# Kernel tuning notes

Measured on AMD Instinct MI355X. Metric: run time of the kernel, lower is better.

Reference implementation:

```python
import jax, jax.numpy as jnp
import numpy as np

D_MODEL, D_K, D_V, H = 1024, 64, 64, 16
B, NQ, NK = 2, 2048, 2048


def setup_inputs() -> dict:
    key = jax.random.key(0)
    ks = jax.random.split(key, 12)
    hd = H * D_K
    xav = lambda k, shape: jax.random.uniform(k, shape, jnp.float32, -1.0, 1.0) * np.sqrt(6.0 / (shape[0] + shape[1]))
    return {
        "queries": jax.random.normal(ks[0], (B, NQ, D_MODEL), jnp.float32),
        "keys": jax.random.normal(ks[1], (B, NK, D_MODEL), jnp.float32),
        "values": jax.random.normal(ks[2], (B, NK, D_MODEL), jnp.float32),
        "memory": jax.random.uniform(ks[3], (B, NK), jnp.float32),
        "Wq": xav(ks[4], (D_MODEL, hd)), "bq": jnp.zeros((hd,), jnp.float32),
        "Wk": xav(ks[5], (D_MODEL, hd)), "bk": jnp.zeros((hd,), jnp.float32),
        "Wv": xav(ks[6], (D_MODEL, H * D_V)), "bv": jnp.zeros((H * D_V,), jnp.float32),
        "Wo": xav(ks[7], (H * D_V, D_MODEL)), "bo": jnp.zeros((D_MODEL,), jnp.float32),
        "Wmm": xav(ks[8], (1, H * D_V)), "bmm": jnp.zeros((H * D_V,), jnp.float32),
    }


def reference(queries, keys, values, memory, Wq, bq, Wk, bk, Wv, bv, Wo, bo, Wmm, bmm):
    b, nq = queries.shape[:2]
    nk = keys.shape[1]
    # projections -> (b, h, n, d)
    q = (queries @ Wq + bq).reshape(b, nq, H, D_K).transpose(0, 2, 1, 3)
    k = (keys @ Wk + bk).reshape(b, nk, H, D_K).transpose(0, 2, 1, 3)
    v = (values @ Wv + bv).reshape(b, nk, H, D_V).transpose(0, 2, 1, 3)
    # memory gate: fc_mm(memory[..., None]) -> (b, nk, h*d_k) -> (b, h, nk, d_k)
    mm = (memory[:, :, None] * Wmm[0] + bmm).reshape(b, nk, H, D_K).transpose(0, 2, 1, 3)
    att = jnp.einsum("bhqd,bhkd->bhqk", q, k * mm) / np.sqrt(D_K).astype(np.float32)
    att = jax.nn.softmax(att, axis=-1)
    out = jnp.einsum("bhqk,bhkd->bhqd", att, v * mm)
    out = out.transpose(0, 2, 1, 3).reshape(b, nq, H * D_V)
    return out @ Wo + bo
```

## Files before the change

### kernel.cpp

```cpp
#include <hip/hip_runtime.h>
#include <hip/hip_bf16.h>

#define H_   16
#define NQ_  2048
#define NK_  2048
#define DM_  1024

typedef float f32x4 __attribute__((ext_vector_type(4)));
typedef float f32x16 __attribute__((ext_vector_type(16)));
typedef __bf16 bf16x8 __attribute__((ext_vector_type(8)));
typedef unsigned short u16x8 __attribute__((ext_vector_type(8)));
typedef unsigned short u16x4 __attribute__((ext_vector_type(4)));

__device__ __forceinline__ unsigned short bfbits(float x) {
  __bf16 h = (__bf16)x;
  return __builtin_bit_cast(unsigned short, h);
}

__global__ __launch_bounds__(256) void prep(
    const float* __restrict__ Wq, const float* __restrict__ Wk,
    const float* __restrict__ Wv, const float* __restrict__ Wo,
    unsigned short* __restrict__ WqT, unsigned short* __restrict__ WkT,
    unsigned short* __restrict__ WvT, unsigned short* __restrict__ WoT,
    const float* __restrict__ q, const float* __restrict__ k, const float* __restrict__ v,
    unsigned short* __restrict__ qo, unsigned short* __restrict__ ko,
    unsigned short* __restrict__ vo) {
  __shared__ float t[64][65];
  const int flat = blockIdx.x;
  if (flat < 1024) {
    const int z = flat >> 8, bx = (flat >> 4) & 15, by = flat & 15;
    const float* src = (z == 0) ? Wq : (z == 1) ? Wk : (z == 2) ? Wv : Wo;
    unsigned short* dst = (z == 0) ? WqT : (z == 1) ? WkT : (z == 2) ? WvT : WoT;
    const int r0 = bx * 64, c0 = by * 64;
    for (int i = threadIdx.x; i < 4096; i += 256) {
      int r = i >> 6, c = i & 63;
      t[r][c] = src[(size_t)(r0 + r) * DM_ + c0 + c];
    }
    __syncthreads();
    for (int i = threadIdx.x; i < 4096; i += 256) {
      int n = i >> 6, kk = i & 63;
      dst[(size_t)(c0 + n) * DM_ + r0 + kk] = bfbits(t[kk][n]);
    }
  } else {
    const int tt = flat - 1024;
    const int which = tt >> 11;
    const float* src = (which == 0) ? q : (which == 1) ? k : v;
    unsigned short* dst = (which == 0) ? qo : (which == 1) ? ko : vo;
    const int i = (tt & 2047) * 256 + threadIdx.x;
    const float4* s4 = (const float4*)src;
    float4 a = s4[2 * i], b = s4[2 * i + 1];
    bf16x8 o;
    o[0] = (__bf16)a.x; o[1] = (__bf16)a.y; o[2] = (__bf16)a.z; o[3] = (__bf16)a.w;
    o[4] = (__bf16)b.x; o[5] = (__bf16)b.y; o[6] = (__bf16)b.z; o[7] = (__bf16)b.w;
    *((bf16x8*)dst + i) = o;
  }
}

__device__ __forceinline__ void gll16(const unsigned short* g, unsigned short* l) {
  __builtin_amdgcn_global_load_lds((const __attribute__((address_space(1))) void*)g,
                                   (__attribute__((address_space(3))) void*)l, 16, 0, 0);
}

template <int MODE>
__device__ __forceinline__ void gemm128_body(
    int bx, int by,
    const unsigned short* __restrict__ A, const unsigned short* __restrict__ Bt, int K,
    const float* __restrict__ bias, const float* __restrict__ mem,
    const float* __restrict__ Wmm, const float* __restrict__ bmm,
    unsigned short* __restrict__ obf,
    unsigned short* Al, unsigned short* Bl) {
  const int tid = threadIdx.x, lane = tid & 63, w = tid >> 6;
  const int wm = w >> 1, wn = w & 1;
  const int m0 = bx * 128, n0 = by * 128;
  const int lrow = lane >> 2, lcol = (lane & 3) * 8;
  const int fr = lane & 15, fk = (lane >> 4) * 8;

  f32x4 acc[4][4] = {};

  const unsigned short* ag0 = A + (size_t)(m0 + w * 32 + lrow) * K + lcol;
  const unsigned short* bg0 = Bt + (size_t)(n0 + w * 32 + lrow) * K + lcol;
  unsigned short* la0 = &Al[(w * 32) * 32];
  unsigned short* la1 = &Al[(w * 32 + 16) * 32];
  unsigned short* lb0 = &Bl[(w * 32) * 32];
  unsigned short* lb1 = &Bl[(w * 32 + 16) * 32];
  const size_t s16K = (size_t)16 * K;

  const int KT = K >> 5;
  for (int kt = 0; kt < KT; ++kt) {
    gll16(ag0, la0); gll16(ag0 + s16K, la1);
    gll16(bg0, lb0); gll16(bg0 + s16K, lb1);
    ag0 += 32; bg0 += 32;
    __syncthreads();
    bf16x8 af[4], bfr[4];
#pragma unroll
    for (int i = 0; i < 4; ++i) af[i] = *(const bf16x8*)&Al[(wm * 64 + i * 16 + fr) * 32 + fk];
#pragma unroll
    for (int j = 0; j < 4; ++j) bfr[j] = *(const bf16x8*)&Bl[(wn * 64 + j * 16 + fr) * 32 + fk];
#pragma unroll
    for (int i = 0; i < 4; ++i)
#pragma unroll
      for (int j = 0; j < 4; ++j)
        acc[i][j] = __builtin_amdgcn_mfma_f32_16x16x32_bf16(af[i], bfr[j], acc[i][j], 0, 0, 0);
    __syncthreads();
  }

#pragma unroll
  for (int i = 0; i < 4; ++i) {
    const int rowb = m0 + wm * 64 + i * 16 + (lane >> 4) * 4;
#pragma unroll
    for (int j = 0; j < 4; ++j) {
      const int col = n0 + wn * 64 + j * 16 + fr;
#pragma unroll
      for (int r = 0; r < 4; ++r) {
        float v = acc[i][j][r];
        int rr = rowb + r;
        if (MODE == 0) {
          int b = rr >> 11, nq = rr & 2047, h = col >> 6, d = col & 63;
          float val = (v + bias[col]) * 0.180336884f;
          obf[(((size_t)(b * H_ + h)) * NQ_ + nq) * 64 + d] = bfbits(val);
        } else if (MODE == 1) {
          int b = rr >> 11, nk = rr & 2047, h = col >> 6, d = col & 63;
          float gate = mem[b * NK_ + nk] * Wmm[col] + bmm[col];
          float val = (v + bias[col]) * gate;
          obf[(((size_t)(b * H_ + h)) * NK_ + nk) * 64 + d] = bfbits(val);
        } else {
          int b = col >> 11, key = col & 2047, h = rr >> 6, d = rr & 63;
          float gate = mem[b * NK_ + key] * Wmm[rr] + bmm[rr];
          float val = (v + bias[rr]) * gate;
          int keyp = (key & ~12) | ((key & 4) << 1) | ((key & 8) >> 1);
          obf[(((size_t)(b * H_ + h)) * 64 + d) * NK_ + keyp] = bfbits(val);
        }
      }
    }
  }
}

__global__ __launch_bounds__(256) void gemm_qkv3(
    const unsigned short* __restrict__ qbf, const unsigned short* __restrict__ kbf,
    const unsigned short* __restrict__ vbf, const unsigned short* __restrict__ WvT,
    const unsigned short* __restrict__ WqT, const unsigned short* __restrict__ WkT,
    const float* __restrict__ bq, const float* __restrict__ bk, const float* __restrict__ bv,
    const float* __restrict__ mem, const float* __restrict__ Wmm, const float* __restrict__ bmm,
    unsigned short* __restrict__ Qp, unsigned short* __restrict__ Kp,
    unsigned short* __restrict__ VpT) {
  __shared__ unsigned short Al[128 * 32];
  __shared__ unsigned short Bl[128 * 32];
  const int gid = (blockIdx.x & 7) * 96 + (blockIdx.x >> 3);
  if (gid < 256) {
    gemm128_body<0>(gid & 31, gid >> 5, qbf, WqT, 1024, bq, nullptr, nullptr, nullptr,
                    Qp, Al, Bl);
  } else if (gid < 512) {
    int bb = gid - 256;
    gemm128_body<1>(bb & 31, bb >> 5, kbf, WkT, 1024, bk, mem, Wmm, bmm, Kp, Al, Bl);
  } else {
    int bb = gid - 512;
    gemm128_body<2>(bb & 7, bb >> 3, WvT, vbf, 1024, bv, mem, Wmm, bmm, VpT, Al, Bl);
  }
}

__global__ __launch_bounds__(256) void gemm_out(
    const unsigned short* __restrict__ AO, const unsigned short* __restrict__ WoT,
    const float* __restrict__ bo, float* __restrict__ out) {
  __shared__ unsigned short Al[64 * 32];
  __shared__ unsigned short Bl[128 * 32];
  const int b = (blockIdx.x & 7) * 64 + (blockIdx.x >> 3);
  const int bx = b & 63, by = b >> 6;
  const int tid = threadIdx.x, lane = tid & 63, w = tid >> 6;
  const int wm = w >> 1, wn = w & 1;
  const int m0 = bx * 64, n0 = by * 128;
  const int lrow = lane >> 2, lcol = (lane & 3) * 8;
  const int fr = lane & 15, fk = (lane >> 4) * 8;
  const int K = 1024;

  f32x4 acc[2][4] = {};

  const unsigned short* ag = AO + (size_t)(m0 + w * 16 + lrow) * K + lcol;
  const unsigned short* bg = WoT + (size_t)(n0 + w * 32 + lrow) * K + lcol;
  unsigned short* la0 = &Al[(w * 16) * 32];
  unsigned short* lb0 = &Bl[(w * 32) * 32];
  unsigned short* lb1 = &Bl[(w * 32 + 16) * 32];
  const size_t s16K = (size_t)16 * K;

  for (int kt = 0; kt < 32; ++kt) {
    gll16(ag, la0);
    gll16(bg, lb0); gll16(bg + s16K, lb1);
    ag += 32; bg += 32;
    __syncthreads();
    bf16x8 af[2], bfr[4];
#pragma unroll
    for (int i = 0; i < 2; ++i) af[i] = *(const bf16x8*)&Al[(wm * 32 + i * 16 + fr) * 32 + fk];
#pragma unroll
    for (int j = 0; j < 4; ++j) bfr[j] = *(const bf16x8*)&Bl[(wn * 64 + j * 16 + fr) * 32 + fk];
#pragma unroll
    for (int i = 0; i < 2; ++i)
#pragma unroll
      for (int j = 0; j < 4; ++j)
        acc[i][j] = __builtin_amdgcn_mfma_f32_16x16x32_bf16(af[i], bfr[j], acc[i][j], 0, 0, 0);
    __syncthreads();
  }

#pragma unroll
  for (int i = 0; i < 2; ++i) {
    const int rowb = m0 + wm * 32 + i * 16 + (lane >> 4) * 4;
#pragma unroll
    for (int j = 0; j < 4; ++j) {
      const int col = n0 + wn * 64 + j * 16 + fr;
#pragma unroll
      for (int r = 0; r < 4; ++r)
        out[(size_t)(rowb + r) * DM_ + col] = acc[i][j][r] + bo[col];
    }
  }
}

__global__ __launch_bounds__(256, 2) void flash_attn(const unsigned short* __restrict__ Qp,
                                                     const unsigned short* __restrict__ Kp,
                                                     const unsigned short* __restrict__ VpT,
                                                     unsigned short* __restrict__ AO) {
  __shared__ unsigned short Ks[2][128][66];
  __shared__ unsigned short Vs[2][64][130];

  const int tid = threadIdx.x, lane = tid & 63, w = tid >> 6;
  const int gid = (blockIdx.x & 7) * 64 + (blockIdx.x >> 3);
  const int bh = gid >> 4;
  const int qt = gid & 15;
  const int r31 = lane & 31, hi2 = lane >> 5;

  const unsigned short* qg = Qp + (((size_t)bh * NQ_) + qt * 128 + w * 32 + r31) * 64 + hi2 * 8;
  bf16x8 qf[4];
#pragma unroll
  for (int s = 0; s < 4; ++s) qf[s] = *(const bf16x8*)&qg[s * 16];

  const int krow = tid >> 1, kcol = (tid & 1) * 32;
  const int vrow = tid >> 2, vcol = (tid & 3) * 32;
  const unsigned short* kg = Kp + ((size_t)bh * NK_ + krow) * 64 + kcol;
  const unsigned short* vg = VpT + ((size_t)bh * 64 + vrow) * NK_ + vcol;

  f32x16 acc0 = {}, acc1 = {};
  float m_run = -1e30f, l_run = 0.0f;

  u16x8 kr[4], vr[4];
#pragma unroll
  for (int i = 0; i < 4; ++i) {
    kr[i] = *(const u16x8*)(kg + 8 * i);
    vr[i] = *(const u16x8*)(vg + 8 * i);
  }
#pragma unroll
  for (int i = 0; i < 4; ++i) {
    *(u16x8*)&Ks[0][krow][kcol + 8 * i] = kr[i];
    *(u16x8*)&Vs[0][vrow][vcol + 8 * i] = vr[i];
  }

  for (int kt = 0; kt < 16; ++kt) {
    const int cur = kt & 1;
    __syncthreads();

    f32x16 sv[4] = {};
    __builtin_amdgcn_s_setprio(1);
#pragma unroll
    for (int s = 0; s < 4; ++s) {
#pragma unroll
      for (int kb = 0; kb < 4; ++kb) {
        bf16x8 ka = *(const bf16x8*)&Ks[cur][kb * 32 + r31][s * 16 + hi2 * 8];
        sv[kb] = __builtin_amdgcn_mfma_f32_32x32x16_bf16(ka, qf[s], sv[kb], 0, 0, 0);
      }
    }
    __builtin_amdgcn_s_setprio(0);

    if (kt + 1 < 16) {
      const unsigned short* kn = kg + (size_t)(kt + 1) * 128 * 64;
      const unsigned short* vn = vg + (kt + 1) * 128;
#pragma unroll
      for (int i = 0; i < 4; ++i) {
        kr[i] = *(const u16x8*)(kn + 8 * i);
        vr[i] = *(const u16x8*)(vn + 8 * i);
      }
    }

    float mxp[4];
#pragma unroll
    for (int kb = 0; kb < 4; ++kb) {
      float m = fmaxf(sv[kb][0], sv[kb][1]);
#pragma unroll
      for (int g = 2; g < 16; ++g) m = fmaxf(m, sv[kb][g]);
      mxp[kb] = m;
    }
    float mx = fmaxf(fmaxf(mxp[0], mxp[1]), fmaxf(mxp[2], mxp[3]));
    mx = fmaxf(mx, __shfl_xor(mx, 32));

    if (__any(mx > m_run + 8.0f)) {
      float mnew = fmaxf(m_run, mx);
      float sc = __builtin_amdgcn_exp2f(m_run - mnew);
      m_run = mnew;
      l_run *= sc;
      acc0 *= sc;
      acc1 *= sc;
    }

    float psp[4] = {0.f, 0.f, 0.f, 0.f};
    bf16x8 pb[8];
#pragma unroll
    for (int kb = 0; kb < 4; ++kb) {
#pragma unroll
      for (int g = 0; g < 16; ++g) {
        float p = __builtin_amdgcn_exp2f(sv[kb][g] - m_run);
        psp[kb] += p;
        pb[2 * kb + (g >> 3)][g & 7] = (__bf16)p;
      }
    }
    float ps = (psp[0] + psp[1]) + (psp[2] + psp[3]);
    ps += __shfl_xor(ps, 32);
    l_run += ps;

    __builtin_amdgcn_s_setprio(1);
#pragma unroll
    for (int ks = 0; ks < 8; ++ks) {
      bf16x8 va0 = *(const bf16x8*)&Vs[cur][r31][ks * 16 + hi2 * 8];
      bf16x8 va1 = *(const bf16x8*)&Vs[cur][32 + r31][ks * 16 + hi2 * 8];
      acc0 = __builtin_amdgcn_mfma_f32_32x32x16_bf16(va0, pb[ks], acc0, 0, 0, 0);
      acc1 = __builtin_amdgcn_mfma_f32_32x32x16_bf16(va1, pb[ks], acc1, 0, 0, 0);
    }
    __builtin_amdgcn_s_setprio(0);

    if (kt + 1 < 16) {
#pragma unroll
      for (int i = 0; i < 4; ++i) {
        *(u16x8*)&Ks[cur ^ 1][krow][kcol + 8 * i] = kr[i];
        *(u16x8*)&Vs[cur ^ 1][vrow][vcol + 8 * i] = vr[i];
      }
    }
  }

  const int b = bh >> 4, h = bh & 15;
  const float linv = 1.0f / l_run;
  const int qrow = qt * 128 + w * 32 + r31;
  const size_t rowbase = (((size_t)b * NQ_ + qrow) << 10) + h * 64;
#pragma unroll
  for (int c = 0; c < 4; ++c) {
    u16x4 o0, o1;
#pragma unroll
    for (int i = 0; i < 4; ++i) {
      o0[i] = bfbits(acc0[c * 4 + i] * linv);
      o1[i] = bfbits(acc1[c * 4 + i] * linv);
    }
    *(u16x4*)&AO[rowbase + 8 * c + 4 * hi2]      = o0;
    *(u16x4*)&AO[rowbase + 32 + 8 * c + 4 * hi2] = o1;
  }
}

extern "C" void kernel_launch(void* const* d_in, const int* in_sizes, int n_in,
                              void* d_out, int out_size, void* d_ws, size_t ws_size,
                              hipStream_t stream) {
  const float* queries = (const float*)d_in[0];
  const float* keys    = (const float*)d_in[1];
  const float* values  = (const float*)d_in[2];
  const float* memory  = (const float*)d_in[3];
  const float* Wq  = (const float*)d_in[4];
  const float* bq  = (const float*)d_in[5];
  const float* Wk  = (const float*)d_in[6];
  const float* bk  = (const float*)d_in[7];
  const float* Wv  = (const float*)d_in[8];
  const float* bv  = (const float*)d_in[9];
  const float* Wo  = (const float*)d_in[10];
  const float* bo  = (const float*)d_in[11];
  const float* Wmm = (const float*)d_in[12];
  const float* bmm = (const float*)d_in[13];

  char* ws = (char*)d_ws;
  const size_t SZ_X = (size_t)4096 * 1024 * 2;
  const size_t SZ_W = (size_t)1024 * 1024 * 2;
  unsigned short* qbf = (unsigned short*)(ws);
  unsigned short* kbf = (unsigned short*)(ws + SZ_X);
  unsigned short* vbf = (unsigned short*)(ws + 2 * SZ_X);
  unsigned short* AO  = (unsigned short*)(ws);
  size_t off = 3 * SZ_X;
  unsigned short* WqT = (unsigned short*)(ws + off); off += SZ_W;
  unsigned short* WkT = (unsigned short*)(ws + off); off += SZ_W;
  unsigned short* WvT = (unsigned short*)(ws + off); off += SZ_W;
  unsigned short* WoT = (unsigned short*)(ws + off); off += SZ_W;
  unsigned short* Qp  = (unsigned short*)(ws + off); off += SZ_X;
  unsigned short* Kp  = (unsigned short*)(ws + off); off += SZ_X;
  unsigned short* VpT = (unsigned short*)(ws + off); off += SZ_X;

  prep<<<7168, 256, 0, stream>>>(Wq, Wk, Wv, Wo, WqT, WkT, WvT, WoT,
                                 queries, keys, values, qbf, kbf, vbf);

  gemm_qkv3<<<768, 256, 0, stream>>>(qbf, kbf, vbf, WvT, WqT, WkT,
                                     bq, bk, bv, memory, Wmm, bmm, Qp, Kp, VpT);

  flash_attn<<<512, 256, 0, stream>>>(Qp, Kp, VpT, AO);

  gemm_out<<<512, 256, 0, stream>>>(AO, WoT, bo, (float*)d_out);
}
```

Baseline: 132.4 us.

## Split attention over two key halves and merge partial outputs

The attention kernel now splits the 2048 keys into two halves processed by separate blocks, which doubles the grid to 1024 blocks. It also halves the K/V shared-memory tile to 64 keys and raises the occupancy hint to 4 blocks per CU. Each block writes an unnormalized bf16 partial output plus its running max and sum. A new merge kernel combines the two halves with log-sum-exp weights. The aim is more parallelism and better latency hiding, paid for by an extra kernel launch, extra partial-output traffic, more barriers per key, and storing unnormalized partials in bf16.

After: 138.8 us. 4.8% more time.

```diff
diff --git a/kernel.cpp b/kernel.cpp
--- a/kernel.cpp
+++ b/kernel.cpp
@@ -15,6 +15,10 @@
 __device__ __forceinline__ unsigned short bfbits(float x) {
   __bf16 h = (__bf16)x;
   return __builtin_bit_cast(unsigned short, h);
+}
+__device__ __forceinline__ float bf2f(unsigned short h) {
+  unsigned int u = ((unsigned int)h) << 16;
+  return __builtin_bit_cast(float, u);
 }
 
 __global__ __launch_bounds__(256) void prep(
@@ -212,17 +216,19 @@
   }
 }
 
-__global__ __launch_bounds__(256, 2) void flash_attn(const unsigned short* __restrict__ Qp,
+__global__ __launch_bounds__(256, 4) void flash_attn(const unsigned short* __restrict__ Qp,
                                                      const unsigned short* __restrict__ Kp,
                                                      const unsigned short* __restrict__ VpT,
-                                                     unsigned short* __restrict__ AO) {
-  __shared__ unsigned short Ks[2][128][66];
-  __shared__ unsigned short Vs[2][64][130];
+                                                     unsigned short* __restrict__ Opart,
+                                                     float* __restrict__ ml) {
+  __shared__ unsigned short Ks[2][64][66];
+  __shared__ unsigned short Vs[2][64][66];
 
   const int tid = threadIdx.x, lane = tid & 63, w = tid >> 6;
-  const int gid = (blockIdx.x & 7) * 64 + (blockIdx.x >> 3);
-  const int bh = gid >> 4;
+  const int gid = (blockIdx.x & 7) * 128 + (blockIdx.x >> 3);
   const int qt = gid & 15;
+  const int bh = (gid >> 4) & 31;
+  const int half = gid >> 9;
   const int r31 = lane & 31, hi2 = lane >> 5;
 
   const unsigned short* qg = Qp + (((size_t)bh * NQ_) + qt * 128 + w * 32 + r31) * 64 + hi2 * 8;
@@ -230,61 +236,44 @@
 #pragma unroll
   for (int s = 0; s < 4; ++s) qf[s] = *(const bf16x8*)&qg[s * 16];
 
-  const int krow = tid >> 1, kcol = (tid & 1) * 32;
-  const int vrow = tid >> 2, vcol = (tid & 3) * 32;
-  const unsigned short* kg = Kp + ((size_t)bh * NK_ + krow) * 64 + kcol;
-  const unsigned short* vg = VpT + ((size_t)bh * 64 + vrow) * NK_ + vcol;
+  const int srow = tid >> 2, scol = (tid & 3) * 16;
+  const unsigned short* kg = Kp + ((size_t)bh * NK_ + half * 1024 + srow) * 64 + scol;
+  const unsigned short* vg = VpT + ((size_t)bh * 64 + srow) * NK_ + half * 1024 + scol;
 
   f32x16 acc0 = {}, acc1 = {};
   float m_run = -1e30f, l_run = 0.0f;
 
-  u16x8 kr[4], vr[4];
-#pragma unroll
-  for (int i = 0; i < 4; ++i) {
-    kr[i] = *(const u16x8*)(kg + 8 * i);
-    vr[i] = *(const u16x8*)(vg + 8 * i);
-  }
-#pragma unroll
-  for (int i = 0; i < 4; ++i) {
-    *(u16x8*)&Ks[0][krow][kcol + 8 * i] = kr[i];
-    *(u16x8*)&Vs[0][vrow][vcol + 8 * i] = vr[i];
-  }
+  u16x8 kr0 = *(const u16x8*)kg, kr1 = *(const u16x8*)(kg + 8);
+  u16x8 vr0 = *(const u16x8*)vg, vr1 = *(const u16x8*)(vg + 8);
+  *(u16x8*)&Ks[0][srow][scol] = kr0; *(u16x8*)&Ks[0][srow][scol + 8] = kr1;
+  *(u16x8*)&Vs[0][srow][scol] = vr0; *(u16x8*)&Vs[0][srow][scol + 8] = vr1;
 
   for (int kt = 0; kt < 16; ++kt) {
     const int cur = kt & 1;
     __syncthreads();
 
-    f32x16 sv[4] = {};
+    f32x16 sv0 = {}, sv1 = {};
     __builtin_amdgcn_s_setprio(1);
 #pragma unroll
     for (int s = 0; s < 4; ++s) {
-#pragma unroll
-      for (int kb = 0; kb < 4; ++kb) {
-        bf16x8 ka = *(const bf16x8*)&Ks[cur][kb * 32 + r31][s * 16 + hi2 * 8];
-        sv[kb] = __builtin_amdgcn_mfma_f32_32x32x16_bf16(ka, qf[s], sv[kb], 0, 0, 0);
-      }
+      bf16x8 ka0 = *(const bf16x8*)&Ks[cur][r31][s * 16 + hi2 * 8];
+      bf16x8 ka1 = *(const bf16x8*)&Ks[cur][32 + r31][s * 16 + hi2 * 8];
+      sv0 = __builtin_amdgcn_mfma_f32_32x32x16_bf16(ka0, qf[s], sv0, 0, 0, 0);
+      sv1 = __builtin_amdgcn_mfma_f32_32x32x16_bf16(ka1, qf[s], sv1, 0, 0, 0);
     }
     __builtin_amdgcn_s_setprio(0);
 
     if (kt + 1 < 16) {
-      const unsigned short* kn = kg + (size_t)(kt + 1) * 128 * 64;
-      const unsigned short* vn = vg + (kt + 1) * 128;
-#pragma unroll
-      for (int i = 0; i < 4; ++i) {
-        kr[i] = *(const u16x8*)(kn + 8 * i);
-        vr[i] = *(const u16x8*)(vn + 8 * i);
-      }
-    }
-
-    float mxp[4];
-#pragma unroll
-    for (int kb = 0; kb < 4; ++kb) {
-      float m = fmaxf(sv[kb][0], sv[kb][1]);
-#pragma unroll
-      for (int g = 2; g < 16; ++g) m = fmaxf(m, sv[kb][g]);
-      mxp[kb] = m;
-    }
-    float mx = fmaxf(fmaxf(mxp[0], mxp[1]), fmaxf(mxp[2], mxp[3]));
+      const unsigned short* kn = kg + (size_t)(kt + 1) * 64 * 64;
+      const unsigned short* vn = vg + (kt + 1) * 64;
+      kr0 = *(const u16x8*)kn; kr1 = *(const u16x8*)(kn + 8);
+      vr0 = *(const u16x8*)vn; vr1 = *(const u16x8*)(vn + 8);
+    }
+
+    float mA = fmaxf(sv0[0], sv0[1]), mB = fmaxf(sv1[0], sv1[1]);
+#pragma unroll
+    for (int g = 2; g < 16; ++g) { mA = fmaxf(mA, sv0[g]); mB = fmaxf(mB, sv1[g]); }
+    float mx = fmaxf(mA, mB);
     mx = fmaxf(mx, __shfl_xor(mx, 32));
 
     if (__any(mx > m_run + 8.0f)) {
@@ -296,24 +285,23 @@
       acc1 *= sc;
     }
 
-    float psp[4] = {0.f, 0.f, 0.f, 0.f};
-    bf16x8 pb[8];
-#pragma unroll
-    for (int kb = 0; kb < 4; ++kb) {
-#pragma unroll
-      for (int g = 0; g < 16; ++g) {
-        float p = __builtin_amdgcn_exp2f(sv[kb][g] - m_run);
-        psp[kb] += p;
-        pb[2 * kb + (g >> 3)][g & 7] = (__bf16)p;
-      }
-    }
-    float ps = (psp[0] + psp[1]) + (psp[2] + psp[3]);
+    float psA = 0.0f, psB = 0.0f;
+    bf16x8 pb[4];
+#pragma unroll
+    for (int g = 0; g < 16; ++g) {
+      float pA = __builtin_amdgcn_exp2f(sv0[g] - m_run);
+      float pB = __builtin_amdgcn_exp2f(sv1[g] - m_run);
+      psA += pA; psB += pB;
+      pb[g >> 3][g & 7] = (__bf16)pA;
+      pb[2 + (g >> 3)][g & 7] = (__bf16)pB;
+    }
+    float ps = psA + psB;
     ps += __shfl_xor(ps, 32);
     l_run += ps;
 
     __builtin_amdgcn_s_setprio(1);
 #pragma unroll
-    for (int ks = 0; ks < 8; ++ks) {
+    for (int ks = 0; ks < 4; ++ks) {
       bf16x8 va0 = *(const bf16x8*)&Vs[cur][r31][ks * 16 + hi2 * 8];
       bf16x8 va1 = *(const bf16x8*)&Vs[cur][32 + r31][ks * 16 + hi2 * 8];
       acc0 = __builtin_amdgcn_mfma_f32_32x32x16_bf16(va0, pb[ks], acc0, 0, 0, 0);
@@ -322,29 +310,54 @@
     __builtin_amdgcn_s_setprio(0);
 
     if (kt + 1 < 16) {
-#pragma unroll
-      for (int i = 0; i < 4; ++i) {
-        *(u16x8*)&Ks[cur ^ 1][krow][kcol + 8 * i] = kr[i];
-        *(u16x8*)&Vs[cur ^ 1][vrow][vcol + 8 * i] = vr[i];
-      }
+      *(u16x8*)&Ks[cur ^ 1][srow][scol] = kr0; *(u16x8*)&Ks[cur ^ 1][srow][scol + 8] = kr1;
+      *(u16x8*)&Vs[cur ^ 1][srow][scol] = vr0; *(u16x8*)&Vs[cur ^ 1][srow][scol + 8] = vr1;
     }
   }
 
   const int b = bh >> 4, h = bh & 15;
-  const float linv = 1.0f / l_run;
   const int qrow = qt * 128 + w * 32 + r31;
-  const size_t rowbase = (((size_t)b * NQ_ + qrow) << 10) + h * 64;
+  unsigned short* ob = Opart + (((size_t)half * 4096 + b * 2048 + qrow) << 10) + h * 64 + 4 * hi2;
 #pragma unroll
   for (int c = 0; c < 4; ++c) {
     u16x4 o0, o1;
 #pragma unroll
     for (int i = 0; i < 4; ++i) {
-      o0[i] = bfbits(acc0[c * 4 + i] * linv);
-      o1[i] = bfbits(acc1[c * 4 + i] * linv);
-    }
-    *(u16x4*)&AO[rowbase + 8 * c + 4 * hi2]      = o0;
-    *(u16x4*)&AO[rowbase + 32 + 8 * c + 4 * hi2] = o1;
-  }
+      o0[i] = bfbits(acc0[c * 4 + i]);
+      o1[i] = bfbits(acc1[c * 4 + i]);
+    }
+    *(u16x4*)(ob + 8 * c) = o0;
+    *(u16x4*)(ob + 32 + 8 * c) = o1;
+  }
+  if (hi2 == 0) {
+    float2 v; v.x = m_run; v.y = l_run;
+    *(float2*)&ml[(((size_t)half * 32 + bh) * 2048 + qrow) * 2] = v;
+  }
+}
+
+__global__ __launch_bounds__(256) void merge_halves(const unsigned short* __restrict__ Opart,
+                                                    const float* __restrict__ ml,
+                                                    unsigned short* __restrict__ AO) {
+  const int i = blockIdx.x * 256 + threadIdx.x;
+  const int row = i >> 7;
+  const int d8 = (i & 127) * 8;
+  const int b = row >> 11, q = row & 2047, h = d8 >> 6;
+  const int bh = b * 16 + h;
+  const unsigned short* p1 = Opart + ((size_t)row << 10) + d8;
+  const unsigned short* p2 = p1 + ((size_t)4096 << 10);
+  float2 ml1 = *(const float2*)&ml[((size_t)bh * 2048 + q) * 2];
+  float2 ml2 = *(const float2*)&ml[(((size_t)32 + bh) * 2048 + q) * 2];
+  float m = fmaxf(ml1.x, ml2.x);
+  float w1 = __builtin_amdgcn_exp2f(ml1.x - m);
+  float w2 = __builtin_amdgcn_exp2f(ml2.x - m);
+  float inv = 1.0f / (ml1.y * w1 + ml2.y * w2);
+  float s1 = w1 * inv, s2 = w2 * inv;
+  u16x8 a = *(const u16x8*)p1;
+  u16x8 c = *(const u16x8*)p2;
+  u16x8 o;
+#pragma unroll
+  for (int j = 0; j < 8; ++j) o[j] = bfbits(bf2f(a[j]) * s1 + bf2f(c[j]) * s2);
+  *(u16x8*)&AO[((size_t)row << 10) + d8] = o;
 }
 
 extern "C" void kernel_launch(void* const* d_in, const int* in_sizes, int n_in,
@@ -366,20 +379,20 @@
   const float* bmm = (const float*)d_in[13];
 
   char* ws = (char*)d_ws;
-  const size_t SZ_X = (size_t)4096 * 1024 * 2;
-  const size_t SZ_W = (size_t)1024 * 1024 * 2;
-  unsigned short* qbf = (unsigned short*)(ws);
-  unsigned short* kbf = (unsigned short*)(ws + SZ_X);
-  unsigned short* vbf = (unsigned short*)(ws + 2 * SZ_X);
-  unsigned short* AO  = (unsigned short*)(ws);
-  size_t off = 3 * SZ_X;
-  unsigned short* WqT = (unsigned short*)(ws + off); off += SZ_W;
-  unsigned short* WkT = (unsigned short*)(ws + off); off += SZ_W;
-  unsigned short* WvT = (unsigned short*)(ws + off); off += SZ_W;
-  unsigned short* WoT = (unsigned short*)(ws + off); off += SZ_W;
-  unsigned short* Qp  = (unsigned short*)(ws + off); off += SZ_X;
-  unsigned short* Kp  = (unsigned short*)(ws + off); off += SZ_X;
-  unsigned short* VpT = (unsigned short*)(ws + off); off += SZ_X;
+  const size_t MB = 1024 * 1024;
+  unsigned short* qbf   = (unsigned short*)(ws);
+  unsigned short* AO    = (unsigned short*)(ws);
+  unsigned short* kbf   = (unsigned short*)(ws + 8 * MB);
+  unsigned short* vbf   = (unsigned short*)(ws + 16 * MB);
+  unsigned short* Opart = (unsigned short*)(ws + 8 * MB);
+  float*          mlb   = (float*)(ws + 24 * MB);
+  unsigned short* WqT   = (unsigned short*)(ws + 26 * MB);
+  unsigned short* WkT   = (unsigned short*)(ws + 28 * MB);
+  unsigned short* WvT   = (unsigned short*)(ws + 30 * MB);
+  unsigned short* WoT   = (unsigned short*)(ws + 32 * MB);
+  unsigned short* Qp    = (unsigned short*)(ws + 34 * MB);
+  unsigned short* Kp    = (unsigned short*)(ws + 42 * MB);
+  unsigned short* VpT   = (unsigned short*)(ws + 50 * MB);
 
   prep<<<7168, 256, 0, stream>>>(Wq, Wk, Wv, Wo, WqT, WkT, WvT, WoT,
                                  queries, keys, values, qbf, kbf, vbf);
@@ -387,7 +400,9 @@
   gemm_qkv3<<<768, 256, 0, stream>>>(qbf, kbf, vbf, WvT, WqT, WkT,
                                      bq, bk, bv, memory, Wmm, bmm, Qp, Kp, VpT);
 
-  flash_attn<<<512, 256, 0, stream>>>(Qp, Kp, VpT, AO);
+  flash_attn<<<1024, 256, 0, stream>>>(Qp, Kp, VpT, Opart, mlb);
+
+  merge_halves<<<2048, 256, 0, stream>>>(Opart, mlb, AO);
 
   gemm_out<<<512, 256, 0, stream>>>(AO, WoT, bo, (float*)d_out);
 }
```

## Double-buffer LDS tiles in projection GEMMs to overlap loads with MFMA

Applied to the files above, without the earlier changes.

Both the QKV projection GEMM and the output GEMM now use two LDS buffers per operand. The next K-tile is fetched with global_load_lds before the MFMAs on the current tile run, so global-memory latency can hide behind compute instead of stalling at a barrier every iteration. This doubles LDS use per block, which may reduce occupancy. Overlap depends on the trailing barrier waiting for the asynchronous loads to finish.

Measured after the change: 128.6 us. -2.9%, faster.

```diff
diff --git a/kernel.cpp b/kernel.cpp
--- a/kernel.cpp
+++ b/kernel.cpp
@@ -74,28 +74,36 @@
   const int m0 = bx * 128, n0 = by * 128;
   const int lrow = lane >> 2, lcol = (lane & 3) * 8;
   const int fr = lane & 15, fk = (lane >> 4) * 8;
+  constexpr int TSZ = 128 * 32;
 
   f32x4 acc[4][4] = {};
 
   const unsigned short* ag0 = A + (size_t)(m0 + w * 32 + lrow) * K + lcol;
   const unsigned short* bg0 = Bt + (size_t)(n0 + w * 32 + lrow) * K + lcol;
-  unsigned short* la0 = &Al[(w * 32) * 32];
-  unsigned short* la1 = &Al[(w * 32 + 16) * 32];
-  unsigned short* lb0 = &Bl[(w * 32) * 32];
-  unsigned short* lb1 = &Bl[(w * 32 + 16) * 32];
+  const int oa0 = (w * 32) * 32, oa1 = (w * 32 + 16) * 32;
   const size_t s16K = (size_t)16 * K;
 
   const int KT = K >> 5;
+  gll16(ag0, Al + oa0); gll16(ag0 + s16K, Al + oa1);
+  gll16(bg0, Bl + oa0); gll16(bg0 + s16K, Bl + oa1);
+  ag0 += 32; bg0 += 32;
+  __syncthreads();
+
   for (int kt = 0; kt < KT; ++kt) {
-    gll16(ag0, la0); gll16(ag0 + s16K, la1);
-    gll16(bg0, lb0); gll16(bg0 + s16K, lb1);
-    ag0 += 32; bg0 += 32;
-    __syncthreads();
+    const int cb = (kt & 1) * TSZ;
+    const int sb = TSZ - cb;
+    if (kt + 1 < KT) {
+      gll16(ag0, Al + sb + oa0); gll16(ag0 + s16K, Al + sb + oa1);
+      gll16(bg0, Bl + sb + oa0); gll16(bg0 + s16K, Bl + sb + oa1);
+      ag0 += 32; bg0 += 32;
+    }
     bf16x8 af[4], bfr[4];
 #pragma unroll
-    for (int i = 0; i < 4; ++i) af[i] = *(const bf16x8*)&Al[(wm * 64 + i * 16 + fr) * 32 + fk];
-#pragma unroll
-    for (int j = 0; j < 4; ++j) bfr[j] = *(const bf16x8*)&Bl[(wn * 64 + j * 16 + fr) * 32 + fk];
+    for (int i = 0; i < 4; ++i)
+      af[i] = *(const bf16x8*)&Al[cb + (wm * 64 + i * 16 + fr) * 32 + fk];
+#pragma unroll
+    for (int j = 0; j < 4; ++j)
+      bfr[j] = *(const bf16x8*)&Bl[cb + (wn * 64 + j * 16 + fr) * 32 + fk];
 #pragma unroll
     for (int i = 0; i < 4; ++i)
 #pragma unroll
@@ -143,8 +151,8 @@
     const float* __restrict__ mem, const float* __restrict__ Wmm, const float* __restrict__ bmm,
     unsigned short* __restrict__ Qp, unsigned short* __restrict__ Kp,
     unsigned short* __restrict__ VpT) {
-  __shared__ unsigned short Al[128 * 32];
-  __shared__ unsigned short Bl[128 * 32];
+  __shared__ unsigned short Al[2 * 128 * 32];
+  __shared__ unsigned short Bl[2 * 128 * 32];
   const int gid = (blockIdx.x & 7) * 96 + (blockIdx.x >> 3);
   if (gid < 256) {
     gemm128_body<0>(gid & 31, gid >> 5, qbf, WqT, 1024, bq, nullptr, nullptr, nullptr,
@@ -161,8 +169,8 @@
 __global__ __launch_bounds__(256) void gemm_out(
     const unsigned short* __restrict__ AO, const unsigned short* __restrict__ WoT,
     const float* __restrict__ bo, float* __restrict__ out) {
-  __shared__ unsigned short Al[64 * 32];
-  __shared__ unsigned short Bl[128 * 32];
+  __shared__ unsigned short Al[2 * 64 * 32];
+  __shared__ unsigned short Bl[2 * 128 * 32];
   const int b = (blockIdx.x & 7) * 64 + (blockIdx.x >> 3);
   const int bx = b & 63, by = b >> 6;
   const int tid = threadIdx.x, lane = tid & 63, w = tid >> 6;
@@ -171,26 +179,36 @@
   const int lrow = lane >> 2, lcol = (lane & 3) * 8;
   const int fr = lane & 15, fk = (lane >> 4) * 8;
   const int K = 1024;
+  constexpr int TA = 64 * 32, TB = 128 * 32;
 
   f32x4 acc[2][4] = {};
 
   const unsigned short* ag = AO + (size_t)(m0 + w * 16 + lrow) * K + lcol;
   const unsigned short* bg = WoT + (size_t)(n0 + w * 32 + lrow) * K + lcol;
-  unsigned short* la0 = &Al[(w * 16) * 32];
-  unsigned short* lb0 = &Bl[(w * 32) * 32];
-  unsigned short* lb1 = &Bl[(w * 32 + 16) * 32];
+  const int oa = (w * 16) * 32;
+  const int ob0 = (w * 32) * 32, ob1 = (w * 32 + 16) * 32;
   const size_t s16K = (size_t)16 * K;
 
+  gll16(ag, Al + oa);
+  gll16(bg, Bl + ob0); gll16(bg + s16K, Bl + ob1);
+  ag += 32; bg += 32;
+  __syncthreads();
+
   for (int kt = 0; kt < 32; ++kt) {
-    gll16(ag, la0);
-    gll16(bg, lb0); gll16(bg + s16K, lb1);
-    ag += 32; bg += 32;
-    __syncthreads();
+    const int ca = (kt & 1) * TA, cbb = (kt & 1) * TB;
+    const int sa = TA - ca, sbb = TB - cbb;
+    if (kt + 1 < 32) {
+      gll16(ag, Al + sa + oa);
+      gll16(bg, Bl + sbb + ob0); gll16(bg + s16K, Bl + sbb + ob1);
+      ag += 32; bg += 32;
+    }
     bf16x8 af[2], bfr[4];
 #pragma unroll
-    for (int i = 0; i < 2; ++i) af[i] = *(const bf16x8*)&Al[(wm * 32 + i * 16 + fr) * 32 + fk];
-#pragma unroll
-    for (int j = 0; j < 4; ++j) bfr[j] = *(const bf16x8*)&Bl[(wn * 64 + j * 16 + fr) * 32 + fk];
+    for (int i = 0; i < 2; ++i)
+      af[i] = *(const bf16x8*)&Al[ca + (wm * 32 + i * 16 + fr) * 32 + fk];
+#pragma unroll
+    for (int j = 0; j < 4; ++j)
+      bfr[j] = *(const bf16x8*)&Bl[cbb + (wn * 64 + j * 16 + fr) * 32 + fk];
 #pragma unroll
     for (int i = 0; i < 2; ++i)
 #pragma unroll
```
